# Kernel tuning notes

Measured on AMD Instinct MI355X. Metric: run time of the kernel, lower is better.

## Reference

```python
import jax, jax.numpy as jnp
import numpy as np

DIM = 768
N_HEADS = 12
HEAD_DIM = DIM // N_HEADS  # 64
SEQ = 4096
ROPE_THETA = 10000.0  # local layer (layer_id=1)
WINDOW = 128          # local_attention; mask is distance <= WINDOW // 2


def setup_inputs() -> dict:
    key = jax.random.key(0)
    k1, k2, k3 = jax.random.split(key, 3)
    x = jax.random.normal(k1, (1, SEQ, DIM), dtype=jnp.float32)
    position_ids = jnp.arange(SEQ, dtype=jnp.int64 if jax.config.jax_enable_x64 else jnp.int32).reshape(1, SEQ)
    wqkv = jax.random.normal(k2, (3 * DIM, DIM), dtype=jnp.float32) * 0.02
    wo = jax.random.normal(k3, (DIM, DIM), dtype=jnp.float32) * 0.02
    return {"x": x, "position_ids": position_ids, "wqkv": wqkv, "wo": wo}


def _rope_cos_sin(position_ids):
    # inv_freq over even dims, freqs duplicated to full head_dim
    inv_freq = 1.0 / (ROPE_THETA ** (jnp.arange(0, HEAD_DIM, 2, dtype=jnp.float32) / HEAD_DIM))
    pos = position_ids.reshape(-1).astype(jnp.float32)           # [S]
    freqs = pos[:, None] * inv_freq[None, :]                      # [S, hd/2]
    freqs = jnp.concatenate([freqs, freqs], axis=-1)              # [S, hd]
    return jnp.cos(freqs)[None, None], jnp.sin(freqs)[None, None]  # [1,1,S,hd]


def _rotate_half(t):
    h = t.shape[-1] // 2
    return jnp.concatenate([-t[..., h:], t[..., :h]], axis=-1)


def reference(x, position_ids, wqkv, wo):
    bsz, seq_len, _ = x.shape
    qkv = jnp.einsum("bsd,ed->bse", x, wqkv)                      # [B,S,3*dim]
    qkv = qkv.reshape(bsz, seq_len, 3, N_HEADS, HEAD_DIM)
    qkv = jnp.transpose(qkv, (0, 3, 2, 1, 4))                      # [B,H,3,S,hd]
    q, k, v = qkv[:, :, 0], qkv[:, :, 1], qkv[:, :, 2]             # [B,H,S,hd]

    cos, sin = _rope_cos_sin(position_ids)
    q = q * cos + _rotate_half(q) * sin
    k = k * cos + _rotate_half(k) * sin

    scale = HEAD_DIM ** -0.5
    scores = jnp.einsum("bhqd,bhkd->bhqk", q, k) * scale           # [B,H,S,S]

    # sliding-window mask: |i - j| <= WINDOW // 2
    idx = jnp.arange(seq_len)
    dist = jnp.abs(idx[None, :] - idx[:, None])                    # [S,S]
    window_mask = dist <= (WINDOW // 2)
    scores = jnp.where(window_mask[None, None], scores, -jnp.inf)

    attn = jax.nn.softmax(scores, axis=-1)
    out = jnp.einsum("bhqk,bhkd->bhqd", attn, v)                   # [B,H,S,hd]
    out = jnp.transpose(out, (0, 2, 1, 3)).reshape(bsz, seq_len, DIM)
    out = jnp.einsum("bsd,ed->bse", out, wo)
    return out
```

## Files before the change

kernel.cpp:

```cpp
#include <hip/hip_runtime.h>
#include <math.h>

#define SEQ 4096
#define DIM 768
#define NH 12
#define HD 64
#define QKV_N 2304
#define HALF_WIN 64

typedef __attribute__((ext_vector_type(8))) short bf16x8;
typedef __attribute__((ext_vector_type(4))) float floatx4;

__device__ __forceinline__ unsigned short f2bf(float f) {
    unsigned u = __float_as_uint(f);
    unsigned r = (u + 0x7fffu + ((u >> 16) & 1u)) >> 16;
    return (unsigned short)r;
}

__device__ __forceinline__ void gld16(const void* g, void* l) {
    __builtin_amdgcn_global_load_lds(
        (const __attribute__((address_space(1))) unsigned*)g,
        (__attribute__((address_space(3))) unsigned*)l, 16, 0, 0);
}

__device__ __forceinline__ void fast_sc(float x, float* s, float* c) {
    float r = x * 0.15915494309189535f;
    r = r - floorf(r);
    *s = __builtin_amdgcn_sinf(r);
    *c = __builtin_amdgcn_cosf(r);
}

__global__ __launch_bounds__(256) void cast3_bf16(const float* __restrict__ x,
                                                  const float* __restrict__ wqkv,
                                                  const float* __restrict__ wo,
                                                  unsigned short* __restrict__ dst,
                                                  int nx4, int nw4, int ntot4) {
    int i = blockIdx.x * 256 + threadIdx.x;
    if (i >= ntot4) return;
    const float4* src;
    int off;
    if (i < nx4)            { src = (const float4*)x;    off = i; }
    else if (i < nx4 + nw4) { src = (const float4*)wqkv; off = i - nx4; }
    else                    { src = (const float4*)wo;   off = i - nx4 - nw4; }
    float4 v = src[off];
    ushort4 r;
    r.x = f2bf(v.x); r.y = f2bf(v.y); r.z = f2bf(v.z); r.w = f2bf(v.w);
    *(ushort4*)(dst + (size_t)i * 4) = r;
}

__global__ __launch_bounds__(256) void gemm_qkv_rope(const unsigned short* __restrict__ A,
                                                     const unsigned short* __restrict__ B,
                                                     unsigned short* __restrict__ qr,
                                                     unsigned short* __restrict__ kr,
                                                     unsigned short* __restrict__ vt) {
    __shared__ __align__(16) short smem[32768];
    const int t  = threadIdx.x;
    const int wv = t >> 6, ln = t & 63;
    const int wm = wv >> 1, wn = wv & 1;
    const int bm0 = blockIdx.y * 128;
    const int bn0 = blockIdx.x * 128;
    const int lrow = ln >> 3;
    const int lu   = ln & 7;
    const int frow = ln & 15;
    const int q    = ln >> 4;
    const int K = DIM;

    const unsigned short* gptr[8];
    int loff[8];
#pragma unroll
    for (int i = 0; i < 8; i++) {
        int idx = wv * 8 + i;
        int c   = (idx < 16) ? idx : idx - 16;
        int row = c * 8 + lrow;
        int g   = (lu ^ (row & 7)) << 3;
        if (idx < 16) {
            gptr[i] = A + (size_t)(bm0 + row) * K + g;
            loff[i] = c * 512;
        } else {
            gptr[i] = B + (size_t)(bn0 + row) * K + g;
            loff[i] = 8192 + c * 512;
        }
    }

    floatx4 acc[4][4];
#pragma unroll
    for (int i = 0; i < 4; i++)
#pragma unroll
        for (int j = 0; j < 4; j++) acc[i][j] = (floatx4){0.f, 0.f, 0.f, 0.f};

#pragma unroll
    for (int i = 0; i < 8; i++) gld16(gptr[i], (void*)(smem + loff[i]));
    __syncthreads();

    int cur = 0;
    for (int it = 0; it < 12; it++) {
        if (it + 1 < 12) {
            int nb = cur ^ 1;
            int k0n = (it + 1) * 64;
#pragma unroll
            for (int i = 0; i < 8; i++)
                gld16(gptr[i] + k0n, (void*)(smem + nb * 16384 + loff[i]));
        }
        short* As = smem + cur * 16384;
        short* Bs = As + 8192;
#pragma unroll
        for (int ks = 0; ks < 2; ks++) {
            bf16x8 af[4], bfr[4];
#pragma unroll
            for (int mt = 0; mt < 4; mt++) {
                int ra = wm * 64 + mt * 16 + frow;
                af[mt] = *(const bf16x8*)&As[ra * 64 + (((ks * 4 + q) ^ (ra & 7)) << 3)];
            }
#pragma unroll
            for (int nt = 0; nt < 4; nt++) {
                int rb = wn * 64 + nt * 16 + frow;
                bfr[nt] = *(const bf16x8*)&Bs[rb * 64 + (((ks * 4 + q) ^ (rb & 7)) << 3)];
            }
#pragma unroll
            for (int mt = 0; mt < 4; mt++)
#pragma unroll
                for (int nt = 0; nt < 4; nt++)
                    acc[mt][nt] = __builtin_amdgcn_mfma_f32_16x16x32_bf16(
                        af[mt], bfr[nt], acc[mt][nt], 0, 0, 0);
        }
        __syncthreads();
        cur ^= 1;
    }

    const int cn = frow;
    const int part = (bn0 >= 1536) ? 2 : (bn0 >= 768 ? 1 : 0);

    if (part < 2) {
        const int wcol = bn0 - part * 768 + wn * 64;
        const int h = wcol >> 6;
        unsigned short* dst = (part == 0 ? qr : kr) + (size_t)h * SEQ * HD;
        const float invf0 = exp2f(-(float)cn * 0.4152410118609203f);
        const float invf1 = exp2f(-(float)(cn + 16) * 0.4152410118609203f);
#pragma unroll
        for (int mt = 0; mt < 4; mt++) {
            const int sbase = bm0 + wm * 64 + mt * 16 + q * 4;
#pragma unroll
            for (int r = 0; r < 4; r++) {
                float ss = (float)(sbase + r);
                float sn0, cs0, sn1, cs1;
                fast_sc(ss * invf0, &sn0, &cs0);
                fast_sc(ss * invf1, &sn1, &cs1);
                float o0 = acc[mt][0][r] * cs0 - acc[mt][2][r] * sn0;
                float o1 = acc[mt][1][r] * cs1 - acc[mt][3][r] * sn1;
                float o2 = acc[mt][2][r] * cs0 + acc[mt][0][r] * sn0;
                float o3 = acc[mt][3][r] * cs1 + acc[mt][1][r] * sn1;
                unsigned short* p = dst + (size_t)(sbase + r) * HD + cn;
                p[0]  = f2bf(o0);
                p[16] = f2bf(o1);
                p[32] = f2bf(o2);
                p[48] = f2bf(o3);
            }
        }
    } else {
        short* vstage = smem + wv * 4608;
#pragma unroll
        for (int mt = 0; mt < 4; mt++) {
#pragma unroll
            for (int nt = 0; nt < 4; nt++) {
                int d    = nt * 16 + cn;
                int sloc = mt * 16 + q * 4;
                ushort4 pk;
                pk.x = f2bf(acc[mt][nt][0]);
                pk.y = f2bf(acc[mt][nt][1]);
                pk.z = f2bf(acc[mt][nt][2]);
                pk.w = f2bf(acc[mt][nt][3]);
                *(ushort4*)&vstage[d * 72 + sloc] = pk;
            }
        }
        __syncthreads();
#pragma unroll
        for (int itr = 0; itr < 8; itr++) {
            int dr = (t >> 4) + itr * 16;
            int u  = t & 15;
            int region = ((u >> 3) << 1) | (dr >> 6);
            uint4 val = *(const uint4*)&smem[region * 4608 + (dr & 63) * 72 + (u & 7) * 8];
            unsigned short* vp = vt + (size_t)(bn0 - 1536 + dr) * SEQ + bm0 + u * 8;
            *(uint4*)vp = val;
        }
    }
}

__global__ __launch_bounds__(256) void gemm_out(const unsigned short* __restrict__ A,
                                                const unsigned short* __restrict__ B,
                                                float* __restrict__ C,
                                                int M, int N, int K) {
    __shared__ __align__(16) short smem[16384];
    const int t  = threadIdx.x;
    const int wv = t >> 6, ln = t & 63;
    const int wm = wv >> 1, wn = wv & 1;
    const int bm0 = blockIdx.y * 64;
    const int bn0 = blockIdx.x * 64;
    const int lrow = ln >> 3;
    const int lu   = ln & 7;
    const int frow = ln & 15;
    const int q    = ln >> 4;

    const unsigned short* gptr[4];
    int loff[4];
#pragma unroll
    for (int i = 0; i < 4; i++) {
        int idx = wv * 4 + i;
        int c   = (idx < 8) ? idx : idx - 8;
        int row = c * 8 + lrow;
        int g   = (lu ^ (row & 7)) << 3;
        if (idx < 8) {
            gptr[i] = A + (size_t)(bm0 + row) * K + g;
            loff[i] = c * 512;
        } else {
            gptr[i] = B + (size_t)(bn0 + row) * K + g;
            loff[i] = 4096 + c * 512;
        }
    }

    floatx4 acc[2][2];
#pragma unroll
    for (int i = 0; i < 2; i++)
#pragma unroll
        for (int j = 0; j < 2; j++) acc[i][j] = (floatx4){0.f, 0.f, 0.f, 0.f};

#pragma unroll
    for (int i = 0; i < 4; i++) gld16(gptr[i], (void*)(smem + loff[i]));
    __syncthreads();

    int cur = 0;
    const int NIT = K / 64;
    for (int it = 0; it < NIT; it++) {
        if (it + 1 < NIT) {
            int nb = cur ^ 1;
            int k0n = (it + 1) * 64;
#pragma unroll
            for (int i = 0; i < 4; i++)
                gld16(gptr[i] + k0n, (void*)(smem + nb * 8192 + loff[i]));
        }
        short* As = smem + cur * 8192;
        short* Bs = As + 4096;
#pragma unroll
        for (int ks = 0; ks < 2; ks++) {
            bf16x8 af[2], bfr[2];
#pragma unroll
            for (int mt = 0; mt < 2; mt++) {
                int ra = wm * 32 + mt * 16 + frow;
                af[mt] = *(const bf16x8*)&As[ra * 64 + (((ks * 4 + q) ^ (ra & 7)) << 3)];
            }
#pragma unroll
            for (int nt = 0; nt < 2; nt++) {
                int rb = wn * 32 + nt * 16 + frow;
                bfr[nt] = *(const bf16x8*)&Bs[rb * 64 + (((ks * 4 + q) ^ (rb & 7)) << 3)];
            }
#pragma unroll
            for (int mt = 0; mt < 2; mt++)
#pragma unroll
                for (int nt = 0; nt < 2; nt++)
                    acc[mt][nt] = __builtin_amdgcn_mfma_f32_16x16x32_bf16(
                        af[mt], bfr[nt], acc[mt][nt], 0, 0, 0);
        }
        __syncthreads();
        cur ^= 1;
    }

    const int cn = ln & 15;
    const int rb4 = (ln >> 4) * 4;
#pragma unroll
    for (int mt = 0; mt < 2; mt++) {
#pragma unroll
        for (int nt = 0; nt < 2; nt++) {
            floatx4 v = acc[mt][nt];
            float* cp = C + (size_t)(bm0 + wm * 32 + mt * 16 + rb4) * N +
                        bn0 + wn * 32 + nt * 16 + cn;
#pragma unroll
            for (int r = 0; r < 4; r++) cp[(size_t)r * N] = v[r];
        }
    }
}

__global__ __launch_bounds__(512) void attn_mfma(const unsigned short* __restrict__ Q,
                                                 const unsigned short* __restrict__ K,
                                                 const unsigned short* __restrict__ Vt,
                                                 unsigned short* __restrict__ Out) {
    __shared__ __align__(16) short lds[24576];
    short* Pb = lds + 16384;
    const int t  = threadIdx.x;
    const int wv = t >> 6, ln = t & 63;
    const int h  = blockIdx.x, qs = blockIdx.y * 128;
    const int frow = ln & 15, qd = ln >> 4;
    const int rl = ln >> 3, uu = ln & 7;
    const unsigned short* Qh = Q + (size_t)h * SEQ * HD;
    const unsigned short* Kh = K + (size_t)h * SEQ * HD;
    const unsigned short* Vh = Vt + (size_t)h * HD * SEQ;

    const unsigned short* qp = Qh + (size_t)(qs + wv * 16 + frow) * HD;
    bf16x8 af0 = *(const bf16x8*)(qp + qd * 8);
    bf16x8 af1 = *(const bf16x8*)(qp + (qd + 4) * 8);

    floatx4 accO[4];
#pragma unroll
    for (int i = 0; i < 4; i++) accO[i] = (floatx4){0.f, 0.f, 0.f, 0.f};
    float m_r[4] = {-1e30f, -1e30f, -1e30f, -1e30f};
    float l_r[4] = {0.f, 0.f, 0.f, 0.f};

    const int qlo = wv * 16;
    const int srow = wv * 8 + rl;
    const int sg   = uu ^ ((srow + (srow >> 3)) & 7);

    {
        const int kb0 = qs - 64;
        const int kbc = kb0 < 0 ? 0 : (kb0 > SEQ - 64 ? SEQ - 64 : kb0);
        gld16(Kh + (size_t)(kbc + srow) * HD + sg * 8, (void*)(lds + wv * 512));
        gld16(Vh + (size_t)srow * SEQ + kbc + sg * 8, (void*)(lds + 4096 + wv * 512));
    }
    __syncthreads();

    int cur = 0;
    for (int c = 0; c < 4; c++) {
        if (c + 1 < 4) {
            const int kb1 = qs - 64 + (c + 1) * 64;
            const int kbc1 = kb1 < 0 ? 0 : (kb1 > SEQ - 64 ? SEQ - 64 : kb1);
            short* nb = lds + (cur ^ 1) * 8192;
            gld16(Kh + (size_t)(kbc1 + srow) * HD + sg * 8, (void*)(nb + wv * 512));
            gld16(Vh + (size_t)srow * SEQ + kbc1 + sg * 8, (void*)(nb + 4096 + wv * 512));
        }
        short* Ks  = lds + cur * 8192;
        short* Vts = Ks + 4096;
        const int kb = qs - 64 + c * 64;

        const int klo0 = c * 64 - 64;
        bool live_kt[4];
        bool any_live = false;
#pragma unroll
        for (int kt = 0; kt < 4; kt++) {
            int d0 = qlo - (klo0 + kt * 16);
            live_kt[kt] = (d0 <= 64) && (d0 >= -64);
            any_live = any_live || live_kt[kt];
        }

        if (any_live) {
            float sv[4][4];
            float cm[4] = {-1e30f, -1e30f, -1e30f, -1e30f};
#pragma unroll
            for (int kt = 0; kt < 4; kt++) {
                if (live_kt[kt]) {
                    int brow = kt * 16 + frow;
                    int bz = (brow + (brow >> 3)) & 7;
                    bf16x8 b0 = *(const bf16x8*)&Ks[brow * 64 + ((qd ^ bz) << 3)];
                    bf16x8 b1 = *(const bf16x8*)&Ks[brow * 64 + (((qd + 4) ^ bz) << 3)];
                    floatx4 z = (floatx4){0.f, 0.f, 0.f, 0.f};
                    z = __builtin_amdgcn_mfma_f32_16x16x32_bf16(af0, b0, z, 0, 0, 0);
                    z = __builtin_amdgcn_mfma_f32_16x16x32_bf16(af1, b1, z, 0, 0, 0);
                    int gk = kb + kt * 16 + frow;
#pragma unroll
                    for (int r = 0; r < 4; r++) {
                        int gq = qs + wv * 16 + qd * 4 + r;
                        int dd = gq - gk;
                        bool valid = (gk >= 0) && (gk < SEQ) &&
                                     (dd <= HALF_WIN) && (dd >= -HALF_WIN);
                        float x = valid ? z[r] * 0.125f : -1e30f;
                        sv[kt][r] = x;
                        cm[r] = fmaxf(cm[r], x);
                    }
                } else {
#pragma unroll
                    for (int r = 0; r < 4; r++) sv[kt][r] = -1e30f;
                }
            }
#pragma unroll
            for (int off = 1; off < 16; off <<= 1)
#pragma unroll
                for (int r = 0; r < 4; r++)
                    cm[r] = fmaxf(cm[r], __shfl_xor(cm[r], off, 64));
            float al[4], ls[4];
#pragma unroll
            for (int r = 0; r < 4; r++) {
                float mn = fmaxf(m_r[r], cm[r]);
                al[r] = __expf(m_r[r] - mn);
                m_r[r] = mn;
                ls[r] = 0.f;
            }
            const int qrb = wv * 16 + qd * 4;
#pragma unroll
            for (int kt = 0; kt < 4; kt++) {
                int klocal = kt * 16 + frow;
                int ku = klocal >> 3;
                if (live_kt[kt]) {
#pragma unroll
                    for (int r = 0; r < 4; r++) {
                        float p = (sv[kt][r] > -1e29f) ? __expf(sv[kt][r] - m_r[r]) : 0.f;
                        ls[r] += p;
                        int qrow = qrb + r;
                        int pz = (qrow + (qrow >> 3)) & 7;
                        Pb[qrow * 64 + ((ku ^ pz) << 3) + (klocal & 7)] = (short)f2bf(p);
                    }
                } else {
#pragma unroll
                    for (int r = 0; r < 4; r++) {
                        int qrow = qrb + r;
                        int pz = (qrow + (qrow >> 3)) & 7;
                        Pb[qrow * 64 + ((ku ^ pz) << 3) + (klocal & 7)] = 0;
                    }
                }
            }
#pragma unroll
            for (int off = 1; off < 16; off <<= 1)
#pragma unroll
                for (int r = 0; r < 4; r++) ls[r] += __shfl_xor(ls[r], off, 64);
#pragma unroll
            for (int r = 0; r < 4; r++) l_r[r] = l_r[r] * al[r] + ls[r];
#pragma unroll
            for (int dt = 0; dt < 4; dt++)
#pragma unroll
                for (int r = 0; r < 4; r++) accO[dt][r] *= al[r];

            const int prow = wv * 16 + frow;
            const int pz2 = (prow + (prow >> 3)) & 7;
            bf16x8 pa0 = *(const bf16x8*)&Pb[prow * 64 + ((qd ^ pz2) << 3)];
            bf16x8 pa1 = *(const bf16x8*)&Pb[prow * 64 + (((qd + 4) ^ pz2) << 3)];
#pragma unroll
            for (int dt = 0; dt < 4; dt++) {
                int vrow = dt * 16 + frow;
                int vz = (vrow + (vrow >> 3)) & 7;
                bf16x8 v0 = *(const bf16x8*)&Vts[vrow * 64 + ((qd ^ vz) << 3)];
                bf16x8 v1 = *(const bf16x8*)&Vts[vrow * 64 + (((qd + 4) ^ vz) << 3)];
                accO[dt] = __builtin_amdgcn_mfma_f32_16x16x32_bf16(pa0, v0, accO[dt], 0, 0, 0);
                accO[dt] = __builtin_amdgcn_mfma_f32_16x16x32_bf16(pa1, v1, accO[dt], 0, 0, 0);
            }
        }
        __syncthreads();
        cur ^= 1;
    }

    short* Ob = lds;
    float linv[4];
#pragma unroll
    for (int r = 0; r < 4; r++) linv[r] = 1.0f / l_r[r];
#pragma unroll
    for (int dt = 0; dt < 4; dt++)
#pragma unroll
        for (int r = 0; r < 4; r++) {
            int qrow = wv * 16 + qd * 4 + r;
            int dcol = dt * 16 + frow;
            Ob[qrow * 72 + dcol] = (short)f2bf(accO[dt][r] * linv[r]);
        }
    __syncthreads();
    const int orow = t >> 2, og = (t & 3) * 16;
    uint4 a = *(const uint4*)&Ob[orow * 72 + og];
    uint4 b = *(const uint4*)&Ob[orow * 72 + og + 8];
    unsigned short* op = Out + (size_t)(qs + orow) * DIM + h * HD + og;
    *(uint4*)(op)     = a;
    *(uint4*)(op + 8) = b;
}

extern "C" void kernel_launch(void* const* d_in, const int* in_sizes, int n_in,
                              void* d_out, int out_size, void* d_ws, size_t ws_size,
                              hipStream_t stream) {
    const float* x    = (const float*)d_in[0];
    const float* wqkv = (const float*)d_in[2];
    const float* wo   = (const float*)d_in[3];
    float* out = (float*)d_out;

    unsigned short* q_r  = (unsigned short*)d_ws;
    unsigned short* k_r  = q_r + (size_t)NH * SEQ * HD;
    unsigned short* v_t  = k_r + (size_t)NH * SEQ * HD;
    unsigned short* x_bf = v_t + (size_t)NH * SEQ * HD;
    unsigned short* wqkv_bf = x_bf + (size_t)SEQ * DIM;
    unsigned short* wo_bf   = wqkv_bf + (size_t)QKV_N * DIM;
    unsigned short* attn_bf = wo_bf + (size_t)DIM * DIM;

    const int nx4 = SEQ * DIM / 4;
    const int nw4 = QKV_N * DIM / 4;
    const int no4 = DIM * DIM / 4;
    const int ntot4 = nx4 + nw4 + no4;

    cast3_bf16<<<dim3((ntot4 + 255) / 256), 256, 0, stream>>>(
        x, wqkv, wo, x_bf, nx4, nw4, ntot4);
    gemm_qkv_rope<<<dim3(QKV_N / 128, SEQ / 128), 256, 0, stream>>>(
        x_bf, wqkv_bf, q_r, k_r, v_t);
    attn_mfma<<<dim3(NH, SEQ / 128), 512, 0, stream>>>(
        q_r, k_r, v_t, attn_bf);
    gemm_out<<<dim3(DIM / 64, SEQ / 64), 256, 0, stream>>>(
        attn_bf, wo_bf, out, SEQ, DIM, DIM);
}
```

Baseline: 127.6 us.

## Use 8 waves per block in QKV GEMM with rope-paired column split

The QKV+RoPE GEMM now runs 512 threads (8 waves) per 128x128 tile instead of 256, and each wave owns a 64x32 sub-tile. Its N fragments are chosen so that each wave holds both halves (d and d+32) of a rotate-half pair, which lets RoPE be applied with one sin/cos per element pair. The V transpose staging is rewritten to a single shared buffer with wider per-thread stores. The aim is more waves to hide latency and lower per-wave register pressure, at the cost of a lower compute-to-LDS-read ratio per wave and more wave scheduling overhead.

```diff
diff --git a/kernel.cpp b/kernel.cpp
--- a/kernel.cpp
+++ b/kernel.cpp
@@ -48,15 +48,16 @@
     *(ushort4*)(dst + (size_t)i * 4) = r;
 }
 
-__global__ __launch_bounds__(256) void gemm_qkv_rope(const unsigned short* __restrict__ A,
-                                                     const unsigned short* __restrict__ B,
-                                                     unsigned short* __restrict__ qr,
-                                                     unsigned short* __restrict__ kr,
-                                                     unsigned short* __restrict__ vt) {
+__global__ __launch_bounds__(512, 4) void gemm_qkv_rope(const unsigned short* __restrict__ A,
+                                                        const unsigned short* __restrict__ B,
+                                                        unsigned short* __restrict__ qr,
+                                                        unsigned short* __restrict__ kr,
+                                                        unsigned short* __restrict__ vt) {
     __shared__ __align__(16) short smem[32768];
     const int t  = threadIdx.x;
     const int wv = t >> 6, ln = t & 63;
-    const int wm = wv >> 1, wn = wv & 1;
+    const int wm = wv >> 2;
+    const int wn = wv & 3;
     const int bm0 = blockIdx.y * 128;
     const int bn0 = blockIdx.x * 128;
     const int lrow = ln >> 3;
@@ -64,12 +65,13 @@
     const int frow = ln & 15;
     const int q    = ln >> 4;
     const int K = DIM;
-
-    const unsigned short* gptr[8];
-    int loff[8];
-#pragma unroll
-    for (int i = 0; i < 8; i++) {
-        int idx = wv * 8 + i;
+    const int nbase = (wn >> 1) * 64 + (wn & 1) * 16;
+
+    const unsigned short* gptr[4];
+    int loff[4];
+#pragma unroll
+    for (int i = 0; i < 4; i++) {
+        int idx = wv * 4 + i;
         int c   = (idx < 16) ? idx : idx - 16;
         int row = c * 8 + lrow;
         int g   = (lu ^ (row & 7)) << 3;
@@ -82,14 +84,14 @@
         }
     }
 
-    floatx4 acc[4][4];
+    floatx4 acc[4][2];
 #pragma unroll
     for (int i = 0; i < 4; i++)
 #pragma unroll
-        for (int j = 0; j < 4; j++) acc[i][j] = (floatx4){0.f, 0.f, 0.f, 0.f};
-
-#pragma unroll
-    for (int i = 0; i < 8; i++) gld16(gptr[i], (void*)(smem + loff[i]));
+        for (int j = 0; j < 2; j++) acc[i][j] = (floatx4){0.f, 0.f, 0.f, 0.f};
+
+#pragma unroll
+    for (int i = 0; i < 4; i++) gld16(gptr[i], (void*)(smem + loff[i]));
     __syncthreads();
 
     int cur = 0;
@@ -98,28 +100,28 @@
             int nb = cur ^ 1;
             int k0n = (it + 1) * 64;
 #pragma unroll
-            for (int i = 0; i < 8; i++)
+            for (int i = 0; i < 4; i++)
                 gld16(gptr[i] + k0n, (void*)(smem + nb * 16384 + loff[i]));
         }
         short* As = smem + cur * 16384;
         short* Bs = As + 8192;
 #pragma unroll
         for (int ks = 0; ks < 2; ks++) {
-            bf16x8 af[4], bfr[4];
+            bf16x8 af[4], bfr[2];
 #pragma unroll
             for (int mt = 0; mt < 4; mt++) {
                 int ra = wm * 64 + mt * 16 + frow;
                 af[mt] = *(const bf16x8*)&As[ra * 64 + (((ks * 4 + q) ^ (ra & 7)) << 3)];
             }
 #pragma unroll
-            for (int nt = 0; nt < 4; nt++) {
-                int rb = wn * 64 + nt * 16 + frow;
+            for (int nt = 0; nt < 2; nt++) {
+                int rb = nbase + nt * 32 + frow;
                 bfr[nt] = *(const bf16x8*)&Bs[rb * 64 + (((ks * 4 + q) ^ (rb & 7)) << 3)];
             }
 #pragma unroll
             for (int mt = 0; mt < 4; mt++)
 #pragma unroll
-                for (int nt = 0; nt < 4; nt++)
+                for (int nt = 0; nt < 2; nt++)
                     acc[mt][nt] = __builtin_amdgcn_mfma_f32_16x16x32_bf16(
                         af[mt], bfr[nt], acc[mt][nt], 0, 0, 0);
         }
@@ -131,57 +133,52 @@
     const int part = (bn0 >= 1536) ? 2 : (bn0 >= 768 ? 1 : 0);
 
     if (part < 2) {
-        const int wcol = bn0 - part * 768 + wn * 64;
-        const int h = wcol >> 6;
+        const int di = (wn & 1) * 16 + cn;
+        const int h  = (bn0 - part * 768 + (wn >> 1) * 64) >> 6;
         unsigned short* dst = (part == 0 ? qr : kr) + (size_t)h * SEQ * HD;
-        const float invf0 = exp2f(-(float)cn * 0.4152410118609203f);
-        const float invf1 = exp2f(-(float)(cn + 16) * 0.4152410118609203f);
+        const float invf = exp2f(-(float)di * 0.4152410118609203f);
 #pragma unroll
         for (int mt = 0; mt < 4; mt++) {
             const int sbase = bm0 + wm * 64 + mt * 16 + q * 4;
 #pragma unroll
             for (int r = 0; r < 4; r++) {
                 float ss = (float)(sbase + r);
-                float sn0, cs0, sn1, cs1;
-                fast_sc(ss * invf0, &sn0, &cs0);
-                fast_sc(ss * invf1, &sn1, &cs1);
-                float o0 = acc[mt][0][r] * cs0 - acc[mt][2][r] * sn0;
-                float o1 = acc[mt][1][r] * cs1 - acc[mt][3][r] * sn1;
-                float o2 = acc[mt][2][r] * cs0 + acc[mt][0][r] * sn0;
-                float o3 = acc[mt][3][r] * cs1 + acc[mt][1][r] * sn1;
-                unsigned short* p = dst + (size_t)(sbase + r) * HD + cn;
-                p[0]  = f2bf(o0);
-                p[16] = f2bf(o1);
-                p[32] = f2bf(o2);
-                p[48] = f2bf(o3);
+                float sn, cs;
+                fast_sc(ss * invf, &sn, &cs);
+                float lo = acc[mt][0][r] * cs - acc[mt][1][r] * sn;
+                float hi = acc[mt][1][r] * cs + acc[mt][0][r] * sn;
+                unsigned short* p = dst + (size_t)(sbase + r) * HD + di;
+                p[0]  = f2bf(lo);
+                p[32] = f2bf(hi);
             }
         }
     } else {
-        short* vstage = smem + wv * 4608;
-#pragma unroll
-        for (int mt = 0; mt < 4; mt++) {
-#pragma unroll
-            for (int nt = 0; nt < 4; nt++) {
-                int d    = nt * 16 + cn;
-                int sloc = mt * 16 + q * 4;
+        short* vstage = smem;
+#pragma unroll
+        for (int nt = 0; nt < 2; nt++) {
+#pragma unroll
+            for (int mt = 0; mt < 4; mt++) {
+                int d    = nbase + nt * 32 + cn;
+                int sloc = wm * 64 + mt * 16 + q * 4;
                 ushort4 pk;
                 pk.x = f2bf(acc[mt][nt][0]);
                 pk.y = f2bf(acc[mt][nt][1]);
                 pk.z = f2bf(acc[mt][nt][2]);
                 pk.w = f2bf(acc[mt][nt][3]);
-                *(ushort4*)&vstage[d * 72 + sloc] = pk;
+                *(ushort4*)&vstage[d * 136 + sloc] = pk;
             }
         }
         __syncthreads();
-#pragma unroll
-        for (int itr = 0; itr < 8; itr++) {
-            int dr = (t >> 4) + itr * 16;
-            int u  = t & 15;
-            int region = ((u >> 3) << 1) | (dr >> 6);
-            uint4 val = *(const uint4*)&smem[region * 4608 + (dr & 63) * 72 + (u & 7) * 8];
-            unsigned short* vp = vt + (size_t)(bn0 - 1536 + dr) * SEQ + bm0 + u * 8;
-            *(uint4*)vp = val;
-        }
+        const int dr = t >> 2, su = (t & 3) * 32;
+        uint4 v0 = *(const uint4*)&vstage[dr * 136 + su];
+        uint4 v1 = *(const uint4*)&vstage[dr * 136 + su + 8];
+        uint4 v2 = *(const uint4*)&vstage[dr * 136 + su + 16];
+        uint4 v3 = *(const uint4*)&vstage[dr * 136 + su + 24];
+        unsigned short* vp = vt + (size_t)(bn0 - 1536 + dr) * SEQ + bm0 + su;
+        *(uint4*)(vp)      = v0;
+        *(uint4*)(vp + 8)  = v1;
+        *(uint4*)(vp + 16) = v2;
+        *(uint4*)(vp + 24) = v3;
     }
 }
 
@@ -476,7 +473,7 @@
 
     cast3_bf16<<<dim3((ntot4 + 255) / 256), 256, 0, stream>>>(
         x, wqkv, wo, x_bf, nx4, nw4, ntot4);
-    gemm_qkv_rope<<<dim3(QKV_N / 128, SEQ / 128), 256, 0, stream>>>(
+    gemm_qkv_rope<<<dim3(QKV_N / 128, SEQ / 128), 512, 0, stream>>>(
         x_bf, wqkv_bf, q_r, k_r, v_t);
     attn_mfma<<<dim3(NH, SEQ / 128), 512, 0, stream>>>(
         q_r, k_r, v_t, attn_bf);
```

After: 128.8 us. No clear change (+1.0%).
